# Performance work log

Hardware: AMD Instinct MI355X
Metric: run time of the kernel (lower is better)

## Reference

```python
import jax, jax.numpy as jnp
import numpy as np

NUM_HEADS = 12
HEAD_DIM = 64
HIDDEN = NUM_HEADS * HEAD_DIM
SCALE = 1.0 / float(np.sqrt(HEAD_DIM))


def _split_heads(x):
    # x: [b, d, s, hidden] -> [b, h, d, s, head_dim]  (transpose_for_scores)
    b, d, s, _ = x.shape
    return jnp.transpose(x.reshape(b, d, s, NUM_HEADS, HEAD_DIM), (0, 3, 1, 2, 4))


def _merge_heads(x):
    # [b, h, d, s, e] -> [b, d, s, hidden]  (untranspose_for_scores)
    b, h, d, s, e = x.shape
    return jnp.transpose(x, (0, 2, 3, 1, 4)).reshape(b, d, s, h * e)


def _segment_attention(q, keys, values, masks, num_docs):
    # _cat_forward: broadcast every key/value/mask list entry to num_docs along
    # dim 2, concat along key length, then scaled-dot-product attention.
    b, h = q.shape[0], q.shape[1]
    q = jnp.broadcast_to(q, (b, h, num_docs, q.shape[3], q.shape[4]))
    k = jnp.concatenate([jnp.broadcast_to(t, (b, h, num_docs, t.shape[3], t.shape[4])) for t in keys], axis=3)
    v = jnp.concatenate([jnp.broadcast_to(t, (b, h, num_docs, t.shape[3], t.shape[4])) for t in values], axis=3)
    mask = jnp.concatenate([jnp.broadcast_to(m, (b, 1, num_docs, 1, m.shape[-1])) for m in masks], axis=-1)
    scores = jnp.einsum('bhdqe,bhdke->bhdqk', q, k) * SCALE + mask
    probs = jax.nn.softmax(scores, axis=-1)
    ctx = jnp.einsum('bhdqk,bhdke->bhdqe', probs, v)
    return _merge_heads(ctx)


def setup_inputs() -> dict:
    key = jax.random.key(0)
    ks = jax.random.split(key, 8)
    B, D, Q, S = 2, 16, 32, 512
    inp = {
        'cls': jax.random.normal(ks[0], (B, 1, 1, HIDDEN), jnp.float32),
        'query': jax.random.normal(ks[1], (B, 1, Q, HIDDEN), jnp.float32),
        'doc': jax.random.normal(ks[2], (B, D, S, HIDDEN), jnp.float32),
        'qmask': jnp.zeros((B, 1, 1, 1, Q), jnp.float32),
        'dmask': jnp.zeros((B, 1, D, 1, S), jnp.float32),
        'Wq': jax.random.normal(ks[3], (HIDDEN, HIDDEN), jnp.float32) * 0.02,
        'bq': jnp.zeros((HIDDEN,), jnp.float32),
        'Wk': jax.random.normal(ks[4], (HIDDEN, HIDDEN), jnp.float32) * 0.02,
        'bk': jnp.zeros((HIDDEN,), jnp.float32),
        'Wv': jax.random.normal(ks[5], (HIDDEN, HIDDEN), jnp.float32) * 0.02,
        'bv': jnp.zeros((HIDDEN,), jnp.float32),
    }
    return inp


def reference(cls, query, doc, qmask, dmask, Wq, bq, Wk, bk, Wv, bv):
    num_docs = doc.shape[1]
    b = cls.shape[0]
    # per-segment q/k/v projections + head split
    segs = {}
    for name, hs in (('cls', cls), ('query', query), ('doc', doc)):
        segs[name] = tuple(_split_heads(hs @ W.T + bb) for W, bb in ((Wq, bq), (Wk, bk), (Wv, bv)))
    cmask = jnp.zeros((b, 1, 1, 1, cls.shape[2]), cls.dtype)  # cls token never padded
    masks = {'cls': cmask, 'query': qmask, 'doc': dmask}
    names = ('cls', 'query', 'doc')
    keys = [segs[n][1] for n in names]
    vals = [segs[n][2] for n in names]
    mlist = [masks[n] for n in names]
    # all segment->segment attention flags default True; attention_window_size
    # is None so each segment goes through the _cat_forward path
    outs = [_segment_attention(segs[n][0], keys, vals, mlist, num_docs) for n in names]
    # cls:[b,D,1,H], query:[b,D,Q,H], doc:[b,D,S,H] -> concat along seq for one output
    return jnp.concatenate(outs, axis=2)
```

## Files before the change

kernel.cpp:

```cpp
#include <hip/hip_runtime.h>
#include <hip/hip_bf16.h>

#define NH      12
#define HD      64
#define HID     768
#define B_      2
#define D_      16
#define QL      32
#define SL      512
#define SEQ     545
#define RPB     8225
#define TOT_ROWS 16450
#define PAD_ROWS 16512
#define VT_R    8256
#define WSZ     589824
#define SCALE_  0.125f
#define LOG2E   1.4426950408889634f
#define QSF     0.18033688011112042f

typedef __attribute__((ext_vector_type(8))) short short8;
typedef __attribute__((ext_vector_type(4))) short short4v;
typedef __attribute__((ext_vector_type(4))) float float4v;
typedef __attribute__((ext_vector_type(2))) unsigned int uint2v;

__device__ __forceinline__ short f2bf(float f) {
    __hip_bfloat16 h = __float2bfloat16(f);
    short s; __builtin_memcpy(&s, &h, 2);
    return s;
}

__device__ __forceinline__ unsigned int cvtpk(float a, float b) {
    unsigned int r;
    asm("v_cvt_pk_bf16_f32 %0, %1, %2" : "=v"(r) : "v"(a), "v"(b));
    return r;
}

__device__ __forceinline__ void gl2lds16(const short* g, short* l) {
    __builtin_amdgcn_global_load_lds(
        (const __attribute__((address_space(1))) void*)g,
        (__attribute__((address_space(3))) void*)l, 16, 0, 0);
}

#define PACK_BLKS  12384
#define WPACK_BLKS 1728

__global__ __launch_bounds__(256) void pack_all(
    const float* __restrict__ cls, const float* __restrict__ query,
    const float* __restrict__ doc,
    const float* __restrict__ Wq, const float* __restrict__ Wk,
    const float* __restrict__ Wv,
    short* __restrict__ X, short* __restrict__ Wb)
{
    int bid = blockIdx.x;
    if (bid < PACK_BLKS) {
        int idx = (bid * 256 + threadIdx.x) * 4;
        int row = idx / HID;
        int col = idx - row * HID;
        float4 v = make_float4(0.f, 0.f, 0.f, 0.f);
        if (row < TOT_ROWS) {
            int b = row / RPB;
            int r = row - b * RPB;
            const float* src;
            if (r == 0)        src = cls   + b * HID + col;
            else if (r < 33)   src = query + ((size_t)(b * QL + (r - 1))) * HID + col;
            else               src = doc   + ((size_t)(b * (D_ * SL) + (r - 33))) * HID + col;
            v = *reinterpret_cast<const float4*>(src);
        }
        short4v o;
        o[0] = f2bf(v.x); o[1] = f2bf(v.y); o[2] = f2bf(v.z); o[3] = f2bf(v.w);
        *reinterpret_cast<short4v*>(X + idx) = o;
    } else {
        int idx = ((bid - PACK_BLKS) * 256 + threadIdx.x) * 4;
        int z = idx / WSZ;
        int r = idx - z * WSZ;
        const float* src = (z == 0 ? Wq : (z == 1 ? Wk : Wv)) + r;
        float sc = (z == 0) ? QSF : 1.0f;
        float4 v = *reinterpret_cast<const float4*>(src);
        short4v o;
        o[0] = f2bf(v.x * sc); o[1] = f2bf(v.y * sc);
        o[2] = f2bf(v.z * sc); o[3] = f2bf(v.w * sc);
        *reinterpret_cast<short4v*>(Wb + idx) = o;
    }
}

__global__ __launch_bounds__(256) void proj4u(
    const short* __restrict__ X, const short* __restrict__ Wb,
    const float* __restrict__ bq, const float* __restrict__ bk,
    const float* __restrict__ bv,
    short* __restrict__ Qb, short* __restrict__ Kb, short* __restrict__ Vt)
{
    __shared__ short Xs[2][128 * 64];
    __shared__ short Ws[2][128 * 64];

    int tid = threadIdx.x, lane = tid & 63, wave = tid >> 6;

    int lin = blockIdx.x + 18 * blockIdx.y;
    {
        const int q = 290, r = 2;
        int xcd = lin & 7, seq = lin >> 3;
        lin = (xcd < r ? xcd * (q + 1) : r * (q + 1) + (xcd - r) * q) + seq;
    }
    int mblk = lin / 18;
    int nz   = lin - mblk * 18;
    int zi   = nz % 3;
    int nblk = nz / 3;
    bool vsw = (zi == 2);
    const short* W = Wb + (size_t)zi * WSZ;
    int m0 = mblk * 128, n0 = nblk * 128;

    int moff = (wave & 1) * 64, noff = (wave >> 1) * 64;
    int lr = lane & 15, lg = lane >> 4;

    const short* xsrc[4];
    const short* wsrc[4];
#pragma unroll
    for (int p = 0; p < 4; ++p) {
        int s = p * 256 + tid;
        int row = s >> 3, c = s & 7;
        int col = (c ^ (row & 7)) * 8;
        xsrc[p] = X + (size_t)(m0 + row) * HID + col;
        wsrc[p] = W + (size_t)(n0 + row) * HID + col;
    }

    float4v acc[4][4];
    for (int mi = 0; mi < 4; ++mi)
        for (int ni = 0; ni < 4; ++ni)
            acc[mi][ni] = (float4v){0.f, 0.f, 0.f, 0.f};

#define PSTAGE(bufi, kt) do {                                               \
    _Pragma("unroll")                                                       \
    for (int p = 0; p < 4; ++p) {                                           \
        gl2lds16(xsrc[p] + (kt) * 64,                                       \
                 &Xs[bufi][(p * 256 + (tid & 0xC0)) * 8]);                  \
        gl2lds16(wsrc[p] + (kt) * 64,                                       \
                 &Ws[bufi][(p * 256 + (tid & 0xC0)) * 8]);                  \
    } } while (0)

    PSTAGE(0, 0);
#pragma unroll
    for (int kt = 0; kt < 12; ++kt) {
        __syncthreads();
        if (kt < 11) PSTAGE((kt + 1) & 1, kt + 1);
        const short* xb = Xs[kt & 1];
        const short* wb = Ws[kt & 1];
        short8 afl[4], afh[4], bfl[4], bfh[4];
        for (int mi = 0; mi < 4; ++mi) {
            int r = moff + mi * 16 + lr;
            int x0 = lg ^ (r & 7);
            afl[mi] = *reinterpret_cast<const short8*>(&xb[r * 64 + x0 * 8]);
            afh[mi] = *reinterpret_cast<const short8*>(&xb[r * 64 + (x0 ^ 4) * 8]);
        }
        for (int ni = 0; ni < 4; ++ni) {
            int r = noff + ni * 16 + lr;
            int x0 = lg ^ (r & 7);
            bfl[ni] = *reinterpret_cast<const short8*>(&wb[r * 64 + x0 * 8]);
            bfh[ni] = *reinterpret_cast<const short8*>(&wb[r * 64 + (x0 ^ 4) * 8]);
        }
        if (!vsw) {
            for (int mi = 0; mi < 4; ++mi)
                for (int ni = 0; ni < 4; ++ni) {
                    acc[mi][ni] = __builtin_amdgcn_mfma_f32_16x16x32_bf16(
                        afl[mi], bfl[ni], acc[mi][ni], 0, 0, 0);
                    acc[mi][ni] = __builtin_amdgcn_mfma_f32_16x16x32_bf16(
                        afh[mi], bfh[ni], acc[mi][ni], 0, 0, 0);
                }
        } else {
            for (int mi = 0; mi < 4; ++mi)
                for (int ni = 0; ni < 4; ++ni) {
                    acc[mi][ni] = __builtin_amdgcn_mfma_f32_16x16x32_bf16(
                        bfl[ni], afl[mi], acc[mi][ni], 0, 0, 0);
                    acc[mi][ni] = __builtin_amdgcn_mfma_f32_16x16x32_bf16(
                        bfh[ni], afh[mi], acc[mi][ni], 0, 0, 0);
                }
        }
    }
#undef PSTAGE

    if (!vsw) {
        short* Y = zi == 0 ? Qb : Kb;
        const float* bias = zi == 0 ? bq : bk;
        float bsc = zi == 0 ? QSF : 1.0f;
        for (int ni = 0; ni < 4; ++ni) {
            int gcol = n0 + noff + ni * 16 + lr;
            float bb = bias[gcol] * bsc;
            for (int mi = 0; mi < 4; ++mi) {
                int growb = m0 + moff + mi * 16 + lg * 4;
                for (int r = 0; r < 4; ++r)
                    Y[(size_t)(growb + r) * HID + gcol] = f2bf(acc[mi][ni][r] + bb);
            }
        }
    } else {
        for (int ni = 0; ni < 4; ++ni) {
            float4 b4 = *reinterpret_cast<const float4*>(&bv[n0 + noff + ni * 16 + lg * 4]);
            const float* bbr = reinterpret_cast<const float*>(&b4);
            for (int mi = 0; mi < 4; ++mi) {
                int grow = m0 + moff + mi * 16 + lr;
                if (grow >= TOT_ROWS) continue;
                int b  = grow >= RPB ? 1 : 0;
                int rb = grow - b * RPB;
                int vr = rb < 33 ? rb : rb + 7;
                size_t cb = ((size_t)(b * HID + n0 + noff + ni * 16 + lg * 4)) * VT_R;
                for (int r = 0; r < 4; ++r)
                    Vt[cb + (size_t)r * VT_R + vr] = f2bf(acc[mi][ni][r] + bbr[r]);
            }
        }
    }
}

__global__ __launch_bounds__(768) void attn6(
    const short* __restrict__ Qb, const short* __restrict__ Kb,
    const short* __restrict__ Vt,
    const float* __restrict__ qmask, const float* __restrict__ dmask,
    float* __restrict__ out)
{
    __shared__ short Ks[3][64 * 64];
    __shared__ short Vs[3][64 * 64];
    __shared__ float maskv[576];

    int tid  = threadIdx.x;
    int lane = tid & 63, wave = tid >> 6;

    int lin = blockIdx.x + 3 * blockIdx.y;
    {
        int xcd = lin & 7, seq = lin >> 3;
        lin = xcd * 144 + seq;
    }
    int hbd = lin / 3;
    int qc  = lin - hbd * 3;
    int h = hbd >> 5, bd = hbd & 31;
    int b = bd >> 4, d = bd & 15;

    int lr = lane & 15, lg = lane >> 4, lk = lg * 8;
    int sidx = wave >> 2, wq = wave & 3;
    int base = b * RPB;
    const short* vbase = Vt + (size_t)(b * HID + h * HD) * VT_R;

    bool stg = tid < 512;
    int loffK = (tid & 0x1C0) * 8;
    const short *kp = Kb, *vp = Vt, *kp8 = Kb, *vp8 = Vt;
    {
        int r = tid >> 3, c = tid & 7;
        int colsw = (c ^ (r & 7)) * 8;
        if (stg) {
            kp  = Kb + (size_t)(base + 33 + d * SL + r) * HID + h * HD + colsw;
            vp  = vbase + (size_t)r * VT_R + 40 + d * SL + colsw;
            int r8 = r > 32 ? 32 : r;
            kp8 = Kb + (size_t)(base + r8) * HID + h * HD + colsw;
            vp8 = vbase + (size_t)r * VT_R + colsw;
        }
    }

#define ALIN(bufi, kt) do { if (stg) {                            \
    gl2lds16(kp + (size_t)(kt) * 64 * HID, &Ks[bufi][loffK]);     \
    gl2lds16(vp + (kt) * 64, &Vs[bufi][loffK]); } } while (0)
#define A8(bufi) do { if (stg) {                                  \
    gl2lds16(kp8, &Ks[bufi][loffK]);                              \
    gl2lds16(vp8, &Vs[bufi][loffK]); } } while (0)

    ALIN(0, 0);
    ALIN(1, 1);

    if (tid < 576) {
        int i = tid;
        float mv;
        if (i < 512)       mv = dmask[(size_t)(b * D_ + d) * SL + i];
        else if (i == 512) mv = 0.f;
        else if (i < 545)  mv = qmask[b * QL + (i - 513)];
        else               mv = -INFINITY;
        maskv[i] = mv * LOG2E;
    }

    short8 bq0, bq1;
    {
        int qtok = qc * 192 + sidx * 64 + wq * 16 + lr;
        int qrow = qtok < 512 ? base + 33 + d * SL + qtok : base + qtok - 512;
        const short* qp = Qb + (size_t)qrow * HID + h * HD + lk;
        bq0 = *reinterpret_cast<const short8*>(qp);
        bq1 = *reinterpret_cast<const short8*>(qp + 32);
    }

    float m_i = -1e30f;
    float lp  = 0.f;
    float4v o[4];
    for (int nt = 0; nt < 4; ++nt) o[nt] = (float4v){0.f, 0.f, 0.f, 0.f};

    __syncthreads();

#pragma unroll
    for (int kt = 0; kt < 9; ++kt) {
        if (kt >= 1) {
            if (kt == 8) { asm volatile("s_waitcnt vmcnt(0)" ::: "memory"); }
            else         { asm volatile("s_waitcnt vmcnt(2)" ::: "memory"); }
            __builtin_amdgcn_s_barrier();
            __builtin_amdgcn_sched_barrier(0);
        }
        if (kt < 6)       ALIN((kt + 2) % 3, kt + 2);
        else if (kt == 6) A8((kt + 2) % 3);

        const short* kb   = Ks[kt % 3];
        const short* vbuf = Vs[kt % 3];

        float p4[4][4];
        short8 kf0[4], kf1[4];
#pragma unroll
        for (int nt = 0; nt < 4; ++nt) {
            int r = nt * 16 + lr;
            int x0 = lg ^ (r & 7);
            kf0[nt] = *reinterpret_cast<const short8*>(&kb[r * 64 + x0 * 8]);
            kf1[nt] = *reinterpret_cast<const short8*>(&kb[r * 64 + (x0 ^ 4) * 8]);
        }
        __builtin_amdgcn_s_setprio(1);
#pragma unroll
        for (int nt = 0; nt < 4; ++nt) {
            float4v z = *reinterpret_cast<const float4v*>(
                &maskv[kt * 64 + nt * 16 + lg * 4]);
            z = __builtin_amdgcn_mfma_f32_16x16x32_bf16(kf0[nt], bq0, z, 0, 0, 0);
            z = __builtin_amdgcn_mfma_f32_16x16x32_bf16(kf1[nt], bq1, z, 0, 0, 0);
            for (int r = 0; r < 4; ++r) p4[nt][r] = z[r];
        }
        __builtin_amdgcn_s_setprio(0);

        float c0 = fmaxf(fmaxf(p4[0][0], p4[0][1]), p4[0][2]);
        float c1 = fmaxf(fmaxf(p4[0][3], p4[1][0]), p4[1][1]);
        float c2 = fmaxf(fmaxf(p4[1][2], p4[1][3]), p4[2][0]);
        float c3 = fmaxf(fmaxf(p4[2][1], p4[2][2]), p4[2][3]);
        float c4 = fmaxf(fmaxf(p4[3][0], p4[3][1]), p4[3][2]);
        float lmax = fmaxf(fmaxf(fmaxf(c0, c1), fmaxf(c2, c3)),
                           fmaxf(c4, p4[3][3]));

        if (__any(lmax > m_i + 8.0f)) {
            float tmx = fmaxf(lmax, __shfl_xor(lmax, 16));
            tmx = fmaxf(tmx, __shfl_xor(tmx, 32));
            float mnew = fmaxf(m_i, tmx);
            float alpha = exp2f(m_i - mnew);
            m_i = mnew;
            lp *= alpha;
            float al[4];
            for (int r = 0; r < 4; ++r) al[r] = __shfl(alpha, lg * 4 + r);
            for (int nt = 0; nt < 4; ++nt)
                for (int r = 0; r < 4; ++r) o[nt][r] *= al[r];
        }

        for (int nt = 0; nt < 4; ++nt)
            for (int r = 0; r < 4; ++r)
                p4[nt][r] = exp2f(p4[nt][r] - m_i);
        float s0 = (p4[0][0] + p4[0][1]) + (p4[0][2] + p4[0][3]);
        float s1 = (p4[1][0] + p4[1][1]) + (p4[1][2] + p4[1][3]);
        float s2 = (p4[2][0] + p4[2][1]) + (p4[2][2] + p4[2][3]);
        float s3 = (p4[3][0] + p4[3][1]) + (p4[3][2] + p4[3][3]);
        lp += (s0 + s1) + (s2 + s3);

        unsigned int wa[4], wbv[4];
        for (int nt = 0; nt < 4; ++nt) {
            wa[nt]  = cvtpk(p4[nt][0], p4[nt][1]);
            wbv[nt] = cvtpk(p4[nt][2], p4[nt][3]);
        }
        uint2v tA01 = __builtin_amdgcn_permlane32_swap(wa[0],  wa[1],  false, false);
        uint2v uA01 = __builtin_amdgcn_permlane16_swap(tA01[0], tA01[1], false, false);
        uint2v tB01 = __builtin_amdgcn_permlane32_swap(wbv[0], wbv[1], false, false);
        uint2v uB01 = __builtin_amdgcn_permlane16_swap(tB01[0], tB01[1], false, false);
        uint2v tA23 = __builtin_amdgcn_permlane32_swap(wa[2],  wa[3],  false, false);
        uint2v uA23 = __builtin_amdgcn_permlane16_swap(tA23[0], tA23[1], false, false);
        uint2v tB23 = __builtin_amdgcn_permlane32_swap(wbv[2], wbv[3], false, false);
        uint2v uB23 = __builtin_amdgcn_permlane16_swap(tB23[0], tB23[1], false, false);

        union { unsigned int u[4]; short8 s8; } A0, A1;
        A0.u[0] = uA01[0]; A0.u[1] = uB01[0]; A0.u[2] = uA01[1]; A0.u[3] = uB01[1];
        A1.u[0] = uA23[0]; A1.u[1] = uB23[0]; A1.u[2] = uA23[1]; A1.u[3] = uB23[1];
        short8 ap0 = A0.s8;
        short8 ap1 = A1.s8;

        __builtin_amdgcn_s_setprio(1);
#pragma unroll
        for (int nt = 0; nt < 4; ++nt) {
            int rd = nt * 16 + lr;
            int x0 = lg ^ (rd & 7);
            short8 bv0 = *reinterpret_cast<const short8*>(&vbuf[rd * 64 + x0 * 8]);
            short8 bv1 = *reinterpret_cast<const short8*>(&vbuf[rd * 64 + (x0 ^ 4) * 8]);
            o[nt] = __builtin_amdgcn_mfma_f32_16x16x32_bf16(ap0, bv0, o[nt], 0, 0, 0);
            o[nt] = __builtin_amdgcn_mfma_f32_16x16x32_bf16(ap1, bv1, o[nt], 0, 0, 0);
        }
        __builtin_amdgcn_s_setprio(0);
    }
#undef ALIN
#undef A8

    {
        float lt = lp;
        lt += __shfl_xor(lt, 16);
        lt += __shfl_xor(lt, 32);
        float li[4];
        for (int r = 0; r < 4; ++r) li[r] = __shfl(lt, lg * 4 + r);
        for (int r = 0; r < 4; ++r) {
            int t = qc * 192 + sidx * 64 + wq * 16 + lg * 4 + r;
            if (t >= SEQ) continue;
            int seq = t < 512 ? 33 + t : (t == 512 ? 0 : t - 512);
            float inv = 1.f / li[r];
            float* op = out + ((size_t)(bd * SEQ + seq)) * HID + h * HD + lr;
            for (int nt = 0; nt < 4; ++nt)
                op[nt * 16] = o[nt][r] * inv;
        }
    }
}

extern "C" void kernel_launch(void* const* d_in, const int* in_sizes, int n_in,
                              void* d_out, int out_size, void* d_ws, size_t ws_size,
                              hipStream_t stream)
{
    const float* cls   = (const float*)d_in[0];
    const float* query = (const float*)d_in[1];
    const float* doc   = (const float*)d_in[2];
    const float* qmask = (const float*)d_in[3];
    const float* dmask = (const float*)d_in[4];
    const float* Wq = (const float*)d_in[5];
    const float* bq = (const float*)d_in[6];
    const float* Wk = (const float*)d_in[7];
    const float* bk = (const float*)d_in[8];
    const float* Wv = (const float*)d_in[9];
    const float* bv = (const float*)d_in[10];
    float* out = (float*)d_out;

    short* X  = (short*)d_ws;
    size_t seg = (size_t)PAD_ROWS * HID;
    short* Qb = X + seg;
    short* Kb = Qb + seg;
    short* Vt = Kb + seg;
    short* Wb = (short*)d_out;

    pack_all<<<dim3(PACK_BLKS + WPACK_BLKS), 256, 0, stream>>>(
        cls, query, doc, Wq, Wk, Wv, X, Wb);
    proj4u<<<dim3(18, 129, 1), 256, 0, stream>>>(X, Wb, bq, bk, bv, Qb, Kb, Vt);
    attn6<<<dim3(3, NH * 32, 1), 768, 0, stream>>>(Qb, Kb, Vt, qmask, dmask, out);
}
```

Baseline: 270.5 us.

## Split attention into 512-thread blocks with five query chunks and double buffering

The attention kernel moves from 768-thread blocks covering 192 query tokens with a 3-stage K/V LDS ring to 512-thread blocks covering 128 tokens, five chunks per head and document. Staging now uses every thread, and the pipeline becomes a 2-buffer double buffer with a plain __syncthreads at the end of each tile instead of explicit vmcnt waits. This gives more, smaller blocks and less LDS per block, which may improve occupancy and load balance across CUs. The cost is K/V tiles loaded more times overall, since each chunk reloads them, and a shallower prefetch depth with a full barrier every iteration.

```diff
diff --git a/kernel.cpp b/kernel.cpp
--- a/kernel.cpp
+++ b/kernel.cpp
@@ -207,61 +207,55 @@
     }
 }
 
-__global__ __launch_bounds__(768) void attn6(
+__global__ __launch_bounds__(512) void attn7(
     const short* __restrict__ Qb, const short* __restrict__ Kb,
     const short* __restrict__ Vt,
     const float* __restrict__ qmask, const float* __restrict__ dmask,
     float* __restrict__ out)
 {
-    __shared__ short Ks[3][64 * 64];
-    __shared__ short Vs[3][64 * 64];
+    __shared__ short Ks[2][64 * 64];
+    __shared__ short Vs[2][64 * 64];
     __shared__ float maskv[576];
 
     int tid  = threadIdx.x;
     int lane = tid & 63, wave = tid >> 6;
 
-    int lin = blockIdx.x + 3 * blockIdx.y;
+    int lin = blockIdx.x + 5 * blockIdx.y;
     {
         int xcd = lin & 7, seq = lin >> 3;
-        lin = xcd * 144 + seq;
-    }
-    int hbd = lin / 3;
-    int qc  = lin - hbd * 3;
+        lin = xcd * 240 + seq;
+    }
+    int hbd = lin / 5;
+    int qc  = lin - hbd * 5;
     int h = hbd >> 5, bd = hbd & 31;
     int b = bd >> 4, d = bd & 15;
 
     int lr = lane & 15, lg = lane >> 4, lk = lg * 8;
-    int sidx = wave >> 2, wq = wave & 3;
     int base = b * RPB;
     const short* vbase = Vt + (size_t)(b * HID + h * HD) * VT_R;
 
-    bool stg = tid < 512;
     int loffK = (tid & 0x1C0) * 8;
-    const short *kp = Kb, *vp = Vt, *kp8 = Kb, *vp8 = Vt;
+    const short *kp, *vp, *kp8, *vp8;
     {
         int r = tid >> 3, c = tid & 7;
         int colsw = (c ^ (r & 7)) * 8;
-        if (stg) {
-            kp  = Kb + (size_t)(base + 33 + d * SL + r) * HID + h * HD + colsw;
-            vp  = vbase + (size_t)r * VT_R + 40 + d * SL + colsw;
-            int r8 = r > 32 ? 32 : r;
-            kp8 = Kb + (size_t)(base + r8) * HID + h * HD + colsw;
-            vp8 = vbase + (size_t)r * VT_R + colsw;
-        }
-    }
-
-#define ALIN(bufi, kt) do { if (stg) {                            \
+        kp  = Kb + (size_t)(base + 33 + d * SL + r) * HID + h * HD + colsw;
+        vp  = vbase + (size_t)r * VT_R + 40 + d * SL + colsw;
+        int r8 = r > 32 ? 32 : r;
+        kp8 = Kb + (size_t)(base + r8) * HID + h * HD + colsw;
+        vp8 = vbase + (size_t)r * VT_R + colsw;
+    }
+
+#define ALIN(bufi, kt) do {                                       \
     gl2lds16(kp + (size_t)(kt) * 64 * HID, &Ks[bufi][loffK]);     \
-    gl2lds16(vp + (kt) * 64, &Vs[bufi][loffK]); } } while (0)
-#define A8(bufi) do { if (stg) {                                  \
+    gl2lds16(vp + (kt) * 64, &Vs[bufi][loffK]); } while (0)
+#define A8(bufi) do {                                             \
     gl2lds16(kp8, &Ks[bufi][loffK]);                              \
-    gl2lds16(vp8, &Vs[bufi][loffK]); } } while (0)
+    gl2lds16(vp8, &Vs[bufi][loffK]); } while (0)
 
     ALIN(0, 0);
-    ALIN(1, 1);
-
-    if (tid < 576) {
-        int i = tid;
+
+    for (int i = tid; i < 576; i += 512) {
         float mv;
         if (i < 512)       mv = dmask[(size_t)(b * D_ + d) * SL + i];
         else if (i == 512) mv = 0.f;
@@ -272,7 +266,7 @@
 
     short8 bq0, bq1;
     {
-        int qtok = qc * 192 + sidx * 64 + wq * 16 + lr;
+        int qtok = qc * 128 + wave * 16 + lr;
         int qrow = qtok < 512 ? base + 33 + d * SL + qtok : base + qtok - 512;
         const short* qp = Qb + (size_t)qrow * HID + h * HD + lk;
         bq0 = *reinterpret_cast<const short8*>(qp);
@@ -288,17 +282,11 @@
 
 #pragma unroll
     for (int kt = 0; kt < 9; ++kt) {
-        if (kt >= 1) {
-            if (kt == 8) { asm volatile("s_waitcnt vmcnt(0)" ::: "memory"); }
-            else         { asm volatile("s_waitcnt vmcnt(2)" ::: "memory"); }
-            __builtin_amdgcn_s_barrier();
-            __builtin_amdgcn_sched_barrier(0);
-        }
-        if (kt < 6)       ALIN((kt + 2) % 3, kt + 2);
-        else if (kt == 6) A8((kt + 2) % 3);
-
-        const short* kb   = Ks[kt % 3];
-        const short* vbuf = Vs[kt % 3];
+        if (kt < 7)       ALIN((kt + 1) & 1, kt + 1);
+        else if (kt == 7) A8((kt + 1) & 1);
+
+        const short* kb   = Ks[kt & 1];
+        const short* vbuf = Vs[kt & 1];
 
         float p4[4][4];
         short8 kf0[4], kf1[4];
@@ -381,6 +369,8 @@
             o[nt] = __builtin_amdgcn_mfma_f32_16x16x32_bf16(ap1, bv1, o[nt], 0, 0, 0);
         }
         __builtin_amdgcn_s_setprio(0);
+
+        if (kt < 8) __syncthreads();
     }
 #undef ALIN
 #undef A8
@@ -392,7 +382,7 @@
         float li[4];
         for (int r = 0; r < 4; ++r) li[r] = __shfl(lt, lg * 4 + r);
         for (int r = 0; r < 4; ++r) {
-            int t = qc * 192 + sidx * 64 + wq * 16 + lg * 4 + r;
+            int t = qc * 128 + wave * 16 + lg * 4 + r;
             if (t >= SEQ) continue;
             int seq = t < 512 ? 33 + t : (t == 512 ? 0 : t - 512);
             float inv = 1.f / li[r];
@@ -430,5 +420,5 @@
     pack_all<<<dim3(PACK_BLKS + WPACK_BLKS), 256, 0, stream>>>(
         cls, query, doc, Wq, Wk, Wv, X, Wb);
     proj4u<<<dim3(18, 129, 1), 256, 0, stream>>>(X, Wb, bq, bk, bv, Qb, Kb, Vt);
-    attn6<<<dim3(3, NH * 32, 1), 768, 0, stream>>>(Qb, Kb, Vt, qmask, dmask, out);
-}
+    attn7<<<dim3(5, NH * 32, 1), 512, 0, stream>>>(Qb, Kb, Vt, qmask, dmask, out);
+}
```

New measurement: 270.6 us. No clear change (+0.0%).
